# Performance work log

Measured on AMD Instinct MI355X. Metric: run time of the kernel, lower is better.

Reference implementation:

```python
import jax, jax.numpy as jnp
import numpy as np

DIM = 512; DEPTH = 2; HEADS = 8; DIM_HEAD = 64; INNER = HEADS * DIM_HEAD
MEM = 16; TOPK = 8; FF = 4 * DIM
NUM_BUCKETS = 32; MAX_DIST = 128
EPS = 1e-5


def _layernorm(x, g, b):
    m = jnp.mean(x, axis=-1, keepdims=True)
    v = jnp.var(x, axis=-1, keepdims=True)
    return (x - m) * jax.lax.rsqrt(v + EPS) * g + b


def _rel_bucket(rel_pos):
    # T5 relative-position bucketing, causal=True (as hardcoded in Encoder)
    num_buckets = NUM_BUCKETS // 2  # 16
    n = -rel_pos
    ret = (n < 0).astype(jnp.int32) * num_buckets
    n = jnp.abs(n)
    max_exact = num_buckets // 2  # 8
    is_small = n < max_exact
    nf = jnp.maximum(n, 1).astype(jnp.float32)  # safe log; masked by is_small where n==0
    val_if_large = max_exact + (
        jnp.log(nf / max_exact) / np.log(MAX_DIST / max_exact) * (num_buckets - max_exact)
    ).astype(jnp.int32)
    val_if_large = jnp.minimum(val_if_large, num_buckets - 1)
    return ret + jnp.where(is_small, n, val_if_large)


def setup_inputs() -> dict:
    key = jax.random.key(0)
    ks = jax.random.split(key, 16)
    B, N = 2, 2048
    w = lambda k, shape, s=0.02: jax.random.normal(k, shape, jnp.float32) * s
    return {
        "x": jax.random.normal(ks[0], (B, N, DIM), jnp.float32),
        "ln1_g": jnp.ones((DEPTH, DIM), jnp.float32),
        "ln1_b": jnp.zeros((DEPTH, DIM), jnp.float32),
        "Wq": w(ks[1], (DEPTH, DIM, INNER)),
        "Wkv": w(ks[2], (DEPTH, DIM, 2 * INNER)),
        "Wo": w(ks[3], (DEPTH, INNER, DIM)),
        "bo": jnp.zeros((DEPTH, DIM), jnp.float32),
        "pre_proj": w(ks[4], (DEPTH, HEADS, HEADS), 1.0),  # torch.randn init
        "mem_k": w(ks[5], (DEPTH, HEADS, MEM, DIM_HEAD), 1.0),
        "mem_v": w(ks[6], (DEPTH, HEADS, MEM, DIM_HEAD), 1.0),
        "ln2_g": jnp.ones((DEPTH, DIM), jnp.float32),
        "ln2_b": jnp.zeros((DEPTH, DIM), jnp.float32),
        "W1": w(ks[7], (DEPTH, DIM, FF)),
        "b1": jnp.zeros((DEPTH, FF), jnp.float32),
        "W2": w(ks[8], (DEPTH, FF, DIM)),
        "b2": jnp.zeros((DEPTH, DIM), jnp.float32),
        "rel_emb": w(ks[9], (NUM_BUCKETS, HEADS)),
    }


def reference(x, ln1_g, ln1_b, Wq, Wkv, Wo, bo, pre_proj, mem_k, mem_v,
              ln2_g, ln2_b, W1, b1, W2, b2, rel_emb):
    B, N, _ = x.shape
    J = N + MEM  # keys include num_mem_kv memory slots
    scale = DIM_HEAD ** -0.5
    # relative position bias, shape (1, H, N, J); same for every layer
    rel = jnp.arange(J)[None, :] - jnp.arange(N)[:, None]
    bias = jnp.transpose(rel_emb[_rel_bucket(rel)], (2, 0, 1))[None]

    for l in range(DEPTH):
        # --- PreNorm(Attention) + residual ---
        h = _layernorm(x, ln1_g[l], ln1_b[l])
        q = (h @ Wq[l]).reshape(B, N, HEADS, DIM_HEAD).transpose(0, 2, 1, 3)
        k, v = jnp.split(h @ Wkv[l], 2, axis=-1)
        k = k.reshape(B, N, HEADS, DIM_HEAD).transpose(0, 2, 1, 3)
        v = v.reshape(B, N, HEADS, DIM_HEAD).transpose(0, 2, 1, 3)
        k = jnp.concatenate([jnp.broadcast_to(mem_k[l], (B, HEADS, MEM, DIM_HEAD)), k], axis=2)
        v = jnp.concatenate([jnp.broadcast_to(mem_v[l], (B, HEADS, MEM, DIM_HEAD)), v], axis=2)
        dots = jnp.einsum('bhid,bhjd->bhij', q, k) * scale
        dots = jnp.einsum('bhij,hk->bkij', dots, pre_proj[l])  # talking heads (pre-softmax)
        dots = dots + bias
        # sparse top-k masking: keep only values >= k-th largest per row
        thr = jax.lax.top_k(dots, TOPK)[0][..., -1:]
        dots = jnp.where(dots < thr, -jnp.inf, dots)
        attn = jax.nn.softmax(dots, axis=-1)
        out = jnp.einsum('bhij,bhjd->bhid', attn, v)
        out = out.transpose(0, 2, 1, 3).reshape(B, N, INNER)
        x = out @ Wo[l] + bo[l] + x
        # --- PreNorm(FeedForward) + residual ---
        h2 = _layernorm(x, ln2_g[l], ln2_b[l])
        x = jax.nn.gelu(h2 @ W1[l] + b1[l], approximate=False) @ W2[l] + b2[l] + x
    return x
```

## Files before the change

kernel.cpp:

```cpp
#include <hip/hip_runtime.h>
#include <cmath>

typedef __bf16 bf16;
typedef __attribute__((ext_vector_type(8))) __bf16 bf16x8;
typedef __attribute__((ext_vector_type(4))) __bf16 bf16x4;
typedef __attribute__((ext_vector_type(4))) float f32x4;

#define NB 2
#define NSEQ 2048
#define NDIM 512
#define NHEADS 8
#define DHEAD 64
#define NMEM 16
#define NJ 2064
#define NJP 2176
#define NFF 2048
#define NROWS (NB*NSEQ)
#define TBL 4111

enum { EPI_QKV = 0, EPI_GELUSPLIT = 1, EPI_RESID = 2 };

__device__ __forceinline__ int xcd_swz(int bid, int n)
{
  const int cpx = n >> 3;
  return (bid & 7) * cpx + (bid >> 3);
}

template<int BM, int BN, int WAVES_M, int WAVES_N, int EPI>
__global__ __launch_bounds__(256)
void gemm_split(const bf16* __restrict__ A, const bf16* __restrict__ B,
                void* __restrict__ Cv, const float* __restrict__ bias,
                void* __restrict__ Cv2, void* __restrict__ Cv3,
                int K, int lda, int ldb, int ldc, int loA, int loB)
{
  constexpr int BK = 32;
  constexpr int WM = BM / WAVES_M;
  constexpr int WN = BN / WAVES_N;
  constexpr int MF = WM / 16;
  constexpr int NF = WN / 16;
  constexpr int AI = (BM * BK * 2) / 4096;
  constexpr int BI = (BN * BK * 2) / 4096;
  __shared__ bf16 Ash[2][BM * BK];
  __shared__ bf16 Asl[2][BM * BK];
  __shared__ bf16 Bsh[2][BN * BK];
  __shared__ bf16 Bsl[2][BN * BK];

  const int bm0 = xcd_swz(blockIdx.x, gridDim.x) * BM;
  const int bn0 = blockIdx.y * BN;
  const int t = threadIdx.x;
  const int wave = t >> 6, lane = t & 63;
  const int wr = wave / WAVES_N, wc = wave % WAVES_N;
  const int sr = t >> 2, sc = t & 3;
  const int frow = lane & 15, fk = (lane >> 4) * 8;

  auto stage = [&](int buf, int k0) {
#pragma unroll
    for (int qi = 0; qi < AI; ++qi) {
      const long long ro = (long long)(bm0 + qi * 64 + sr) * lda + (k0 + sc * 8);
      __builtin_amdgcn_global_load_lds(
          (const __attribute__((address_space(1))) void*)(A + ro),
          (__attribute__((address_space(3))) void*)(&Ash[buf][qi * 2048 + wave * 512]), 16, 0, 0);
      __builtin_amdgcn_global_load_lds(
          (const __attribute__((address_space(1))) void*)(A + ro + loA),
          (__attribute__((address_space(3))) void*)(&Asl[buf][qi * 2048 + wave * 512]), 16, 0, 0);
    }
#pragma unroll
    for (int qi = 0; qi < BI; ++qi) {
      const long long ro = (long long)(bn0 + qi * 64 + sr) * ldb + (k0 + sc * 8);
      __builtin_amdgcn_global_load_lds(
          (const __attribute__((address_space(1))) void*)(B + ro),
          (__attribute__((address_space(3))) void*)(&Bsh[buf][qi * 2048 + wave * 512]), 16, 0, 0);
      __builtin_amdgcn_global_load_lds(
          (const __attribute__((address_space(1))) void*)(B + ro + loB),
          (__attribute__((address_space(3))) void*)(&Bsl[buf][qi * 2048 + wave * 512]), 16, 0, 0);
    }
  };

  f32x4 acc[MF][NF] = {};

  stage(0, 0);
  __syncthreads();
  int cur = 0;
  for (int k0 = 0; k0 < K; k0 += BK) {
    if (k0 + BK < K) stage(cur ^ 1, k0 + BK);
    bf16x8 afh[MF], afl[MF], bfh[NF], bfl[NF];
#pragma unroll
    for (int m = 0; m < MF; m++) {
      afh[m] = *(const bf16x8*)(&Ash[cur][(wr * WM + m * 16 + frow) * BK + fk]);
      afl[m] = *(const bf16x8*)(&Asl[cur][(wr * WM + m * 16 + frow) * BK + fk]);
    }
#pragma unroll
    for (int n = 0; n < NF; n++) {
      bfh[n] = *(const bf16x8*)(&Bsh[cur][(wc * WN + n * 16 + frow) * BK + fk]);
      bfl[n] = *(const bf16x8*)(&Bsl[cur][(wc * WN + n * 16 + frow) * BK + fk]);
    }
#pragma unroll
    for (int m = 0; m < MF; m++)
#pragma unroll
      for (int n = 0; n < NF; n++) {
        acc[m][n] = __builtin_amdgcn_mfma_f32_16x16x32_bf16(afh[m], bfh[n], acc[m][n], 0, 0, 0);
        acc[m][n] = __builtin_amdgcn_mfma_f32_16x16x32_bf16(afl[m], bfh[n], acc[m][n], 0, 0, 0);
        acc[m][n] = __builtin_amdgcn_mfma_f32_16x16x32_bf16(afh[m], bfl[n], acc[m][n], 0, 0, 0);
      }
    __syncthreads();
    cur ^= 1;
  }

#pragma unroll
  for (int m = 0; m < MF; m++) {
#pragma unroll
    for (int n = 0; n < NF; n++) {
      const int row0 = bm0 + wr * WM + m * 16 + (lane >> 4) * 4;
      const int col = bn0 + wc * WN + n * 16 + (lane & 15);
#pragma unroll
      for (int r = 0; r < 4; r++) {
        const float v = acc[m][n][r];
        const long long i = row0 + r;
        if (EPI == EPI_QKV) {
          const int bb = (int)(i >> 11);
          const int il = (int)(i & 2047);
          if (col < NDIM) {
            const float vq = v * 0.125f;
            bf16* base = (bf16*)Cv;
            const long long ih = i * (long long)(2 * NDIM) + col;
            bf16 h = (bf16)vq;
            base[ih] = h;
            base[ih + NDIM] = (bf16)(vq - (float)h);
          } else if (col < 2 * NDIM) {
            bf16* ks = (bf16*)Cv3;
            const long long ih = ((long long)bb * NJP + il + NMEM) * (long long)(2 * NDIM)
                               + (col - NDIM);
            bf16 h = (bf16)v;
            ks[ih] = h;
            ks[ih + NDIM] = (bf16)(v - (float)h);
          } else {
            ((float*)Cv2)[i * (long long)NDIM + (col - 2 * NDIM)] = v;
          }
        } else if (EPI == EPI_GELUSPLIT) {
          float u = v + bias[col];
          float gl = 0.5f * u * (1.0f + erff(u * 0.7071067811865476f));
          const long long ih = i * (long long)(2 * ldc) + col;
          bf16 h = (bf16)gl;
          ((bf16*)Cv)[ih] = h;
          ((bf16*)Cv)[ih + ldc] = (bf16)(gl - (float)h);
        } else {
          float* xp = ((float*)Cv) + i * ldc + col;
          *xp = *xp + v + bias[col];
        }
      }
    }
  }
}

__global__ __launch_bounds__(256)
void s_gemm_direct(const bf16* __restrict__ Qs, const bf16* __restrict__ Ks,
                   float* __restrict__ S)
{
  const int h = blockIdx.z;
  const int bm0 = xcd_swz(blockIdx.x, gridDim.x) * 128;
  const int bn0 = blockIdx.y * 128;
  const int t = threadIdx.x;
  const int wave = t >> 6, lane = t & 63;
  const int wr = wave >> 1, wc = wave & 1;
  const int frow = lane & 15, fk = (lane >> 4) * 8;

  bf16x8 ah[4][2], al[4][2];
#pragma unroll
  for (int m = 0; m < 4; m++)
#pragma unroll
    for (int kk = 0; kk < 2; kk++) {
      const bf16* ap = Qs + (long long)(bm0 + wr * 64 + m * 16 + frow) * 1024
                     + h * 64 + kk * 32 + fk;
      ah[m][kk] = *(const bf16x8*)(ap);
      al[m][kk] = *(const bf16x8*)(ap + 512);
    }

  f32x4 acc[4][4] = {};
#pragma unroll
  for (int n = 0; n < 4; n++) {
    bf16x8 bh[2], bl[2];
#pragma unroll
    for (int kk = 0; kk < 2; kk++) {
      const bf16* bp = Ks + (long long)(bn0 + wc * 64 + n * 16 + frow) * 1024
                     + h * 64 + kk * 32 + fk;
      bh[kk] = *(const bf16x8*)(bp);
      bl[kk] = *(const bf16x8*)(bp + 512);
    }
#pragma unroll
    for (int m = 0; m < 4; m++)
#pragma unroll
      for (int kk = 0; kk < 2; kk++) {
        acc[m][n] = __builtin_amdgcn_mfma_f32_16x16x32_bf16(ah[m][kk], bh[kk], acc[m][n], 0, 0, 0);
        acc[m][n] = __builtin_amdgcn_mfma_f32_16x16x32_bf16(al[m][kk], bh[kk], acc[m][n], 0, 0, 0);
        acc[m][n] = __builtin_amdgcn_mfma_f32_16x16x32_bf16(ah[m][kk], bl[kk], acc[m][n], 0, 0, 0);
      }
  }

#pragma unroll
  for (int m = 0; m < 4; m++) {
#pragma unroll
    for (int n = 0; n < 4; n++) {
      const int row0 = bm0 + wr * 64 + m * 16 + (lane >> 4) * 4;
      const int col = bn0 + wc * 64 + n * 16 + (lane & 15);
#pragma unroll
      for (int r = 0; r < 4; r++)
        S[(long long)(row0 + r) * (NHEADS * NJP) + h * NJP + col] = acc[m][n][r];
    }
  }
}

__global__ __launch_bounds__(256)
void ln_kernel(const float* __restrict__ x, const float* __restrict__ g,
               const float* __restrict__ b, bf16* __restrict__ out)
{
  const int row = blockIdx.x * 4 + (threadIdx.x >> 6);
  const int lane = threadIdx.x & 63;
  const float* xr = x + (long long)row * NDIM;
  float4 a0 = ((const float4*)xr)[lane];
  float4 a1 = ((const float4*)xr)[lane + 64];
  float s = a0.x + a0.y + a0.z + a0.w + a1.x + a1.y + a1.z + a1.w;
  float ss = a0.x * a0.x + a0.y * a0.y + a0.z * a0.z + a0.w * a0.w
           + a1.x * a1.x + a1.y * a1.y + a1.z * a1.z + a1.w * a1.w;
#pragma unroll
  for (int d = 1; d < 64; d <<= 1) {
    s += __shfl_xor(s, d, 64);
    ss += __shfl_xor(ss, d, 64);
  }
  const float mean = s * (1.0f / NDIM);
  const float var = ss * (1.0f / NDIM) - mean * mean;
  const float rs = rsqrtf(var + 1e-5f);
  float4 g0 = ((const float4*)g)[lane], g1 = ((const float4*)g)[lane + 64];
  float4 b0 = ((const float4*)b)[lane], b1 = ((const float4*)b)[lane + 64];
  bf16* orow = out + (long long)row * (2 * NDIM);
  float y[8] = {
    (a0.x - mean) * rs * g0.x + b0.x, (a0.y - mean) * rs * g0.y + b0.y,
    (a0.z - mean) * rs * g0.z + b0.z, (a0.w - mean) * rs * g0.w + b0.w,
    (a1.x - mean) * rs * g1.x + b1.x, (a1.y - mean) * rs * g1.y + b1.y,
    (a1.z - mean) * rs * g1.z + b1.z, (a1.w - mean) * rs * g1.w + b1.w };
  bf16x4 h0, h1, l0, l1;
#pragma unroll
  for (int j = 0; j < 4; j++) {
    bf16 h = (bf16)y[j];      h0[j] = h;  l0[j] = (bf16)(y[j] - (float)h);
    bf16 h2 = (bf16)y[4 + j]; h1[j] = h2; l1[j] = (bf16)(y[4 + j] - (float)h2);
  }
  *(bf16x4*)(orow + lane * 4) = h0;
  *(bf16x4*)(orow + 256 + lane * 4) = h1;
  *(bf16x4*)(orow + 512 + lane * 4) = l0;
  *(bf16x4*)(orow + 768 + lane * 4) = l1;
}

__global__ __launch_bounds__(256)
void ks_edges(const float* __restrict__ mem_k_l, bf16* __restrict__ Ks)
{
  const int idx = blockIdx.x * 256 + threadIdx.x;
  const int c = idx & 511;
  const int jj = (idx >> 9) & 127;
  const int bb = idx >> 16;
  const int j = (jj < NMEM) ? jj : (jj - NMEM + NJ);
  float kval = 0.f;
  if (jj < NMEM) kval = mem_k_l[((c >> 6) * NMEM + jj) * DHEAD + (c & 63)];
  bf16 hv = (bf16)kval;
  const long long ro = ((long long)bb * NJP + j) * (2 * NDIM) + c;
  Ks[ro] = hv;
  Ks[ro + NDIM] = (bf16)(kval - (float)hv);
}

__global__ __launch_bounds__(512)
void mix_topk_gather(const float* __restrict__ S, const float* __restrict__ kvV,
                     const float* __restrict__ mem_v_l, const float* __restrict__ pp,
                     const float* __restrict__ table2, bf16* __restrict__ obufs,
                     int b)
{
  const int i = blockIdx.x;
  const int k = threadIdx.x >> 6;
  const int lane = threadIdx.x & 63;
  const float* srow = S + (long long)i * (NHEADS * NJP);

  float pk[8];
#pragma unroll
  for (int h = 0; h < 8; h++) pk[h] = pp[h * 8 + k];
  const float* t2k = table2 + k * TBL + (2047 - i);

  float v[34];
#pragma unroll
  for (int t = 0; t < 8; t++) {
    const int j0 = 256 * t + 4 * lane;
    v[4 * t + 0] = t2k[j0];
    v[4 * t + 1] = t2k[j0 + 1];
    v[4 * t + 2] = t2k[j0 + 2];
    v[4 * t + 3] = t2k[j0 + 3];
  }
  {
    const int j0 = 2048 + 2 * lane;
    const int jc = j0 < 2062 ? j0 : 2062;
    v[32] = t2k[jc];
    v[33] = t2k[jc + 1];
  }

#pragma unroll
  for (int h = 0; h < 8; h++) {
    const float* sp = srow + h * NJP;
    const float w = pk[h];
#pragma unroll
    for (int t = 0; t < 8; t++) {
      const float4 s4 = *(const float4*)(sp + 256 * t + 4 * lane);
      v[4 * t + 0] = fmaf(s4.x, w, v[4 * t + 0]);
      v[4 * t + 1] = fmaf(s4.y, w, v[4 * t + 1]);
      v[4 * t + 2] = fmaf(s4.z, w, v[4 * t + 2]);
      v[4 * t + 3] = fmaf(s4.w, w, v[4 * t + 3]);
    }
    const float2 s2 = *(const float2*)(sp + 2048 + 2 * lane);
    v[32] = fmaf(s2.x, w, v[32]);
    v[33] = fmaf(s2.y, w, v[33]);
  }
  {
    const int j0 = 2048 + 2 * lane;
    if (j0 >= NJ) v[32] = -1e30f;
    if (j0 + 1 >= NJ) v[33] = -1e30f;
  }

  float t8[8];
#pragma unroll
  for (int m = 0; m < 8; m++) t8[m] = -3.0e38f;
#pragma unroll
  for (int e = 0; e < 34; e++) {
    float x = v[e];
#pragma unroll
    for (int m = 0; m < 8; m++) {
      const float hi = fmaxf(t8[m], x);
      x = fminf(t8[m], x);
      t8[m] = hi;
    }
  }

#pragma unroll
  for (int d = 1; d < 64; d <<= 1) {
    float o[8], m8[8];
#pragma unroll
    for (int m = 0; m < 8; m++) o[m] = __shfl_xor(t8[m], d, 64);
#pragma unroll
    for (int m = 0; m < 8; m++) m8[m] = fmaxf(t8[m], o[7 - m]);
#define CX(a, bq) { float hi = fmaxf(m8[a], m8[bq]); float lo = fminf(m8[a], m8[bq]); m8[a] = hi; m8[bq] = lo; }
    CX(0, 4) CX(1, 5) CX(2, 6) CX(3, 7)
    CX(0, 2) CX(1, 3) CX(4, 6) CX(5, 7)
    CX(0, 1) CX(2, 3) CX(4, 5) CX(6, 7)
#undef CX
#pragma unroll
    for (int m = 0; m < 8; m++) t8[m] = m8[m];
  }
  const float mx = t8[0];
  const float thr = t8[7];
  float denom = 0.f;
#pragma unroll
  for (int m = 0; m < 8; m++) denom += __expf(t8[m] - mx);
  const float inv = 1.0f / denom;

  float acc = 0.f;
#pragma unroll
  for (int t = 0; t < 8; t++) {
#pragma unroll
    for (int e = 0; e < 4; e++) {
      unsigned long long mball = __ballot(v[t * 4 + e] >= thr);
      while (mball) {
        const int l = __builtin_ctzll(mball);
        mball &= mball - 1;
        const int jj = 256 * t + 4 * l + e;
        const float sv = __shfl(v[t * 4 + e], l);
        const float w = __expf(sv - mx) * inv;
        const float vv = (jj < NMEM)
            ? mem_v_l[(k * NMEM + jj) * DHEAD + lane]
            : kvV[(long long)(b * NSEQ + (jj - NMEM)) * NDIM + k * DHEAD + lane];
        acc = fmaf(w, vv, acc);
      }
    }
  }
#pragma unroll
  for (int e = 0; e < 2; e++) {
    unsigned long long mball = __ballot(v[32 + e] >= thr);
    while (mball) {
      const int l = __builtin_ctzll(mball);
      mball &= mball - 1;
      const int jj = 2048 + 2 * l + e;
      const float sv = __shfl(v[32 + e], l);
      const float w = __expf(sv - mx) * inv;
      const float vv = (jj < NMEM)
          ? mem_v_l[(k * NMEM + jj) * DHEAD + lane]
          : kvV[(long long)(b * NSEQ + (jj - NMEM)) * NDIM + k * DHEAD + lane];
      acc = fmaf(w, vv, acc);
    }
  }

  const long long orow = (long long)(b * NSEQ + i) * (2 * NDIM) + k * DHEAD + lane;
  bf16 h = (bf16)acc;
  obufs[orow] = h;
  obufs[orow + NDIM] = (bf16)(acc - (float)h);
}

__global__ __launch_bounds__(256)
void transpose_split(const float* __restrict__ in, bf16* __restrict__ out,
                     int R, int C)
{
  const long long idx = (long long)blockIdx.x * 256 + threadIdx.x;
  if (idx >= (long long)R * C) return;
  const int r = (int)(idx / C);
  const int c = (int)(idx % C);
  float v = in[idx];
  bf16 h = (bf16)v;
  out[(long long)c * (2 * R) + r] = h;
  out[(long long)c * (2 * R) + R + r] = (bf16)(v - (float)h);
}

__global__ __launch_bounds__(256)
void build_bias2(const float* __restrict__ rel_emb, float* __restrict__ table2)
{
  const int idx = blockIdx.x * 256 + threadIdx.x;
  if (idx >= 8 * TBL) return;
  const int k = idx / TBL;
  const int rel = (idx % TBL) - 2047;
  const int n = -rel;
  const int ret = (n < 0) ? 16 : 0;
  const int na = n < 0 ? -n : n;
  int bucket;
  if (na < 8) {
    bucket = ret + na;
  } else {
    int vl = 8 + (int)(log2((double)na * 0.125) * 2.0);
    vl = vl < 15 ? vl : 15;
    bucket = ret + vl;
  }
  table2[idx] = rel_emb[bucket * 8 + k];
}

extern "C" void kernel_launch(void* const* d_in, const int* in_sizes, int n_in,
                              void* d_out, int out_size, void* d_ws, size_t ws_size,
                              hipStream_t stream)
{
  const float* x_in    = (const float*)d_in[0];
  const float* ln1_g   = (const float*)d_in[1];
  const float* ln1_b   = (const float*)d_in[2];
  const float* Wq      = (const float*)d_in[3];
  const float* Wkv     = (const float*)d_in[4];
  const float* Wo      = (const float*)d_in[5];
  const float* bo      = (const float*)d_in[6];
  const float* pre_proj= (const float*)d_in[7];
  const float* mem_k   = (const float*)d_in[8];
  const float* mem_v   = (const float*)d_in[9];
  const float* ln2_g   = (const float*)d_in[10];
  const float* ln2_b   = (const float*)d_in[11];
  const float* W1      = (const float*)d_in[12];
  const float* b1      = (const float*)d_in[13];
  const float* W2      = (const float*)d_in[14];
  const float* b2      = (const float*)d_in[15];
  const float* rel_emb = (const float*)d_in[16];

  char* p = (char*)d_ws;
  auto alloc = [&](size_t bytes) -> char* {
    char* r = p;
    p += (bytes + 255) & ~(size_t)255;
    return r;
  };

  float* x    = (float*)alloc((size_t)NROWS * NDIM * 4);
  char*  RA   = alloc((size_t)NROWS * 2 * NDIM * 2);
  bf16*  hs    = (bf16*)RA;
  bf16*  obufs = (bf16*)RA;
  char*  RB   = alloc((size_t)NROWS * 2 * NFF * 2);
  bf16*  Qs    = (bf16*)RB;
  bf16*  Ks    = (bf16*)(RB + (size_t)NROWS * 2 * NDIM * 2);
  bf16*  tbufs = (bf16*)RB;
  float* kvV  = (float*)alloc((size_t)NROWS * NDIM * 4);
  float* S    = (float*)alloc((size_t)NSEQ * NHEADS * NJP * 4);
  bf16*  WqkvT= (bf16*)alloc((size_t)2 * 3 * NDIM * 2 * NDIM * 2);
  bf16*  WoT  = (bf16*)alloc((size_t)2 * NDIM * 2 * NDIM * 2);
  bf16*  W1T  = (bf16*)alloc((size_t)2 * NFF * 2 * NDIM * 2);
  bf16*  W2T  = (bf16*)alloc((size_t)2 * NDIM * 2 * NFF * 2);
  float* table2= (float*)alloc((size_t)8 * TBL * 4);

  hipMemcpyAsync(x, x_in, (size_t)NROWS * NDIM * 4, hipMemcpyDeviceToDevice, stream);
  build_bias2<<<(8 * TBL + 255) / 256, 256, 0, stream>>>(rel_emb, table2);
  for (int l = 0; l < 2; l++) {
    bf16* WqkvT_l = WqkvT + (size_t)l * 3 * NDIM * 2 * NDIM;
    transpose_split<<<(NDIM * NDIM + 255) / 256, 256, 0, stream>>>(
        Wq + (size_t)l * NDIM * NDIM, WqkvT_l, NDIM, NDIM);
    transpose_split<<<(2 * NDIM * NDIM + 255) / 256, 256, 0, stream>>>(
        Wkv + (size_t)l * NDIM * 2 * NDIM, WqkvT_l + (size_t)NDIM * 2 * NDIM,
        NDIM, 2 * NDIM);
    transpose_split<<<(NDIM * NDIM + 255) / 256, 256, 0, stream>>>(
        Wo + (size_t)l * NDIM * NDIM, WoT + (size_t)l * NDIM * 2 * NDIM, NDIM, NDIM);
    transpose_split<<<(NDIM * NFF + 255) / 256, 256, 0, stream>>>(
        W1 + (size_t)l * NDIM * NFF, W1T + (size_t)l * NFF * 2 * NDIM, NDIM, NFF);
    transpose_split<<<(NFF * NDIM + 255) / 256, 256, 0, stream>>>(
        W2 + (size_t)l * NFF * NDIM, W2T + (size_t)l * NDIM * 2 * NFF, NFF, NDIM);
  }

  for (int l = 0; l < 2; l++) {
    const bf16* WqkvT_l = WqkvT + (size_t)l * 3 * NDIM * 2 * NDIM;
    const bf16* WoT_l  = WoT + (size_t)l * NDIM * 2 * NDIM;
    const bf16* W1T_l  = W1T + (size_t)l * NFF * 2 * NDIM;
    const bf16* W2T_l  = W2T + (size_t)l * NDIM * 2 * NFF;
    const float* mem_v_l = mem_v + (size_t)l * NHEADS * NMEM * DHEAD;

    ln_kernel<<<NROWS / 4, 256, 0, stream>>>(x, ln1_g + l * NDIM, ln1_b + l * NDIM, hs);
    gemm_split<128, 128, 2, 2, EPI_QKV><<<dim3(NROWS / 128, 12), 256, 0, stream>>>(
        hs, WqkvT_l, Qs, nullptr, kvV, Ks, NDIM, 2 * NDIM, 2 * NDIM, 0, NDIM, NDIM);
    ks_edges<<<(2 * 128 * 512) / 256, 256, 0, stream>>>(
        mem_k + (size_t)l * NHEADS * NMEM * DHEAD, Ks);

    for (int b = 0; b < NB; b++) {
      s_gemm_direct<<<dim3(NSEQ / 128, NJP / 128, NHEADS), 256, 0, stream>>>(
          Qs + (long long)b * NSEQ * 1024, Ks + (long long)b * NJP * 1024, S);
      mix_topk_gather<<<NSEQ, 512, 0, stream>>>(
          S, kvV, mem_v_l, pre_proj + l * 64, table2, obufs, b);
    }

    gemm_split<128, 64, 2, 2, EPI_RESID><<<dim3(NROWS / 128, NDIM / 64), 256, 0, stream>>>(
        obufs, WoT_l, x, bo + l * NDIM, nullptr, nullptr,
        NDIM, 2 * NDIM, 2 * NDIM, NDIM, NDIM, NDIM);

    ln_kernel<<<NROWS / 4, 256, 0, stream>>>(x, ln2_g + l * NDIM, ln2_b + l * NDIM, hs);
    gemm_split<128, 128, 2, 2, EPI_GELUSPLIT><<<dim3(NROWS / 128, NFF / 128), 256, 0, stream>>>(
        hs, W1T_l, tbufs, b1 + l * NFF, nullptr, nullptr,
        NDIM, 2 * NDIM, 2 * NDIM, NFF, NDIM, NDIM);
    gemm_split<128, 64, 2, 2, EPI_RESID><<<dim3(NROWS / 128, NDIM / 64), 256, 0, stream>>>(
        tbufs, W2T_l, x, b2 + l * NDIM, nullptr, nullptr,
        NFF, 2 * NFF, 2 * NFF, NDIM, NFF, NFF);
  }

  hipMemcpyAsync(d_out, x, (size_t)out_size * 4, hipMemcpyDeviceToDevice, stream);
}
```

Baseline: 889.8 us.

## Fuse QK^T score GEMM with talking-heads mix and top-k into one kernel

```diff
diff --git a/kernel.cpp b/kernel.cpp
--- a/kernel.cpp
+++ b/kernel.cpp
@@ -17,6 +17,7 @@
 #define NFF 2048
 #define NROWS (NB*NSEQ)
 #define TBL 4111
+#define JQ 544
 
 enum { EPI_QKV = 0, EPI_GELUSPLIT = 1, EPI_RESID = 2 };
 
@@ -152,61 +153,186 @@
   }
 }
 
-__global__ __launch_bounds__(256)
-void s_gemm_direct(const bf16* __restrict__ Qs, const bf16* __restrict__ Ks,
-                   float* __restrict__ S)
-{
-  const int h = blockIdx.z;
-  const int bm0 = xcd_swz(blockIdx.x, gridDim.x) * 128;
-  const int bn0 = blockIdx.y * 128;
-  const int t = threadIdx.x;
-  const int wave = t >> 6, lane = t & 63;
-  const int wr = wave >> 1, wc = wave & 1;
+__global__ __launch_bounds__(512)
+void attn_fused(const bf16* __restrict__ Qs, const bf16* __restrict__ Ks,
+                const float* __restrict__ pp, const float* __restrict__ table2,
+                float* __restrict__ cand_v, int* __restrict__ cand_i)
+{
+  __shared__ float sS[8 * 64 * 36];
+  const int it = blockIdx.x;
+  const int q  = blockIdx.y;
+  const int b  = blockIdx.z;
+  const int wv = threadIdx.x >> 6;
+  const int lane = threadIdx.x & 63;
+  const int i0 = it * 64;
+  const int jq0 = q * JQ;
+
+  const bf16* Qb = Qs + ((long long)b * NSEQ + i0) * 1024;
+  const bf16* Kb = Ks + (long long)b * NJP * 1024;
   const int frow = lane & 15, fk = (lane >> 4) * 8;
 
   bf16x8 ah[4][2], al[4][2];
 #pragma unroll
   for (int m = 0; m < 4; m++)
 #pragma unroll
-    for (int kk = 0; kk < 2; kk++) {
-      const bf16* ap = Qs + (long long)(bm0 + wr * 64 + m * 16 + frow) * 1024
-                     + h * 64 + kk * 32 + fk;
-      ah[m][kk] = *(const bf16x8*)(ap);
-      al[m][kk] = *(const bf16x8*)(ap + 512);
-    }
-
-  f32x4 acc[4][4] = {};
-#pragma unroll
-  for (int n = 0; n < 4; n++) {
-    bf16x8 bh[2], bl[2];
-#pragma unroll
-    for (int kk = 0; kk < 2; kk++) {
-      const bf16* bp = Ks + (long long)(bn0 + wc * 64 + n * 16 + frow) * 1024
-                     + h * 64 + kk * 32 + fk;
-      bh[kk] = *(const bf16x8*)(bp);
-      bl[kk] = *(const bf16x8*)(bp + 512);
-    }
+    for (int ks = 0; ks < 2; ks++) {
+      const bf16* ap = Qb + (long long)(m * 16 + frow) * 1024 + wv * 64 + ks * 32 + fk;
+      ah[m][ks] = *(const bf16x8*)(ap);
+      al[m][ks] = *(const bf16x8*)(ap + 512);
+    }
+
+  float pk[8];
+#pragma unroll
+  for (int h = 0; h < 8; h++) pk[h] = pp[h * 8 + wv];
+  const float* t2l = table2 + wv * TBL + 2047 - (i0 + lane);
+
+  float t8[8]; int i8[8];
+#pragma unroll
+  for (int m = 0; m < 8; m++) { t8[m] = -3.0e38f; i8[m] = 0; }
+
+  bf16x8 bh[2][2], bl[2][2];
+  auto loadB = [&](int st) {
+    const int j0 = jq0 + st * 32;
+#pragma unroll
+    for (int n = 0; n < 2; n++)
+#pragma unroll
+      for (int ks = 0; ks < 2; ks++) {
+        const bf16* bp = Kb + (long long)(j0 + n * 16 + frow) * 1024 + wv * 64 + ks * 32 + fk;
+        bh[n][ks] = *(const bf16x8*)(bp);
+        bl[n][ks] = *(const bf16x8*)(bp + 512);
+      }
+  };
+  loadB(0);
+
+  for (int st = 0; st < 17; ++st) {
+    f32x4 acc[4][2] = {};
+#pragma unroll
+    for (int n = 0; n < 2; n++)
+#pragma unroll
+      for (int m = 0; m < 4; m++)
+#pragma unroll
+        for (int ks = 0; ks < 2; ks++) {
+          acc[m][n] = __builtin_amdgcn_mfma_f32_16x16x32_bf16(ah[m][ks], bh[n][ks], acc[m][n], 0, 0, 0);
+          acc[m][n] = __builtin_amdgcn_mfma_f32_16x16x32_bf16(al[m][ks], bh[n][ks], acc[m][n], 0, 0, 0);
+          acc[m][n] = __builtin_amdgcn_mfma_f32_16x16x32_bf16(ah[m][ks], bl[n][ks], acc[m][n], 0, 0, 0);
+        }
 #pragma unroll
     for (int m = 0; m < 4; m++)
 #pragma unroll
-      for (int kk = 0; kk < 2; kk++) {
-        acc[m][n] = __builtin_amdgcn_mfma_f32_16x16x32_bf16(ah[m][kk], bh[kk], acc[m][n], 0, 0, 0);
-        acc[m][n] = __builtin_amdgcn_mfma_f32_16x16x32_bf16(al[m][kk], bh[kk], acc[m][n], 0, 0, 0);
-        acc[m][n] = __builtin_amdgcn_mfma_f32_16x16x32_bf16(ah[m][kk], bl[kk], acc[m][n], 0, 0, 0);
+      for (int n = 0; n < 2; n++)
+#pragma unroll
+        for (int r = 0; r < 4; r++)
+          sS[wv * 2304 + (m * 16 + (lane >> 4) * 4 + r) * 36 + n * 16 + (lane & 15)] = acc[m][n][r];
+    __syncthreads();
+
+    if (st < 16) loadB(st + 1);
+
+#pragma unroll
+    for (int s = 0; s < 8; ++s) {
+      const int jl = s * 4;
+      const int jg = jq0 + st * 32 + jl;
+      float v[4];
+#pragma unroll
+      for (int e = 0; e < 4; e++) {
+        const int jr = (jg + e < NJ) ? (jg + e) : (NJ - 1);
+        v[e] = t2l[jr];
       }
-  }
-
-#pragma unroll
-  for (int m = 0; m < 4; m++) {
-#pragma unroll
-    for (int n = 0; n < 4; n++) {
-      const int row0 = bm0 + wr * 64 + m * 16 + (lane >> 4) * 4;
-      const int col = bn0 + wc * 64 + n * 16 + (lane & 15);
-#pragma unroll
-      for (int r = 0; r < 4; r++)
-        S[(long long)(row0 + r) * (NHEADS * NJP) + h * NJP + col] = acc[m][n][r];
-    }
-  }
+#pragma unroll
+      for (int h = 0; h < 8; h++) {
+        const float4 s4 = *(const float4*)(sS + h * 2304 + lane * 36 + jl);
+        v[0] = fmaf(s4.x, pk[h], v[0]);
+        v[1] = fmaf(s4.y, pk[h], v[1]);
+        v[2] = fmaf(s4.z, pk[h], v[2]);
+        v[3] = fmaf(s4.w, pk[h], v[3]);
+      }
+#pragma unroll
+      for (int e = 0; e < 4; e++) {
+        if (jg + e >= NJ) v[e] = -1e30f;
+        const float x = v[e];
+        if (x > t8[7]) {
+          t8[7] = x; i8[7] = jg + e;
+#pragma unroll
+          for (int m = 6; m >= 0; m--)
+            if (t8[m + 1] > t8[m]) {
+              float tv = t8[m]; t8[m] = t8[m + 1]; t8[m + 1] = tv;
+              int ti = i8[m]; i8[m] = i8[m + 1]; i8[m + 1] = ti;
+            }
+        }
+      }
+    }
+    __syncthreads();
+  }
+
+  const long long cb = (((long long)(b * NSEQ + i0 + lane)) * NHEADS + wv) * 32 + q * 8;
+#pragma unroll
+  for (int m = 0; m < 8; m++) {
+    cand_v[cb + m] = t8[m];
+    cand_i[cb + m] = i8[m];
+  }
+}
+
+__global__ __launch_bounds__(512)
+void merge_gather(const float* __restrict__ cand_v, const int* __restrict__ cand_i,
+                  const float* __restrict__ kvV, const float* __restrict__ mem_v_l,
+                  bf16* __restrict__ obufs)
+{
+  const int i = blockIdx.x;
+  const int b = blockIdx.y;
+  const int k = threadIdx.x >> 6;
+  const int lane = threadIdx.x & 63;
+  const long long cbase = (((long long)(b * NSEQ + i)) * NHEADS + k) * 32;
+
+  float cv = -3.0e38f;
+  int ci = 0;
+  if (lane < 32) {
+    cv = cand_v[cbase + lane];
+    ci = cand_i[cbase + lane];
+  }
+
+  float t8[8];
+  t8[0] = cv;
+#pragma unroll
+  for (int m = 1; m < 8; m++) t8[m] = -3.0e38f;
+#pragma unroll
+  for (int d = 1; d < 64; d <<= 1) {
+    float o[8], m8[8];
+#pragma unroll
+    for (int m = 0; m < 8; m++) o[m] = __shfl_xor(t8[m], d, 64);
+#pragma unroll
+    for (int m = 0; m < 8; m++) m8[m] = fmaxf(t8[m], o[7 - m]);
+#define CX(a, bq) { float hi = fmaxf(m8[a], m8[bq]); float lo = fminf(m8[a], m8[bq]); m8[a] = hi; m8[bq] = lo; }
+    CX(0, 4) CX(1, 5) CX(2, 6) CX(3, 7)
+    CX(0, 2) CX(1, 3) CX(4, 6) CX(5, 7)
+    CX(0, 1) CX(2, 3) CX(4, 5) CX(6, 7)
+#undef CX
+#pragma unroll
+    for (int m = 0; m < 8; m++) t8[m] = m8[m];
+  }
+  const float mx = t8[0];
+  const float thr = t8[7];
+  float denom = 0.f;
+#pragma unroll
+  for (int m = 0; m < 8; m++) denom += __expf(t8[m] - mx);
+  const float inv = 1.0f / denom;
+
+  float acc = 0.f;
+  unsigned long long mball = __ballot(cv >= thr);
+  while (mball) {
+    const int l = __builtin_ctzll(mball);
+    mball &= mball - 1;
+    const int jj = __shfl(ci, l);
+    const float sv = __shfl(cv, l);
+    const float w = __expf(sv - mx) * inv;
+    const float vv = (jj < NMEM)
+        ? mem_v_l[(k * NMEM + jj) * DHEAD + lane]
+        : kvV[(long long)(b * NSEQ + (jj - NMEM)) * NDIM + k * DHEAD + lane];
+    acc = fmaf(w, vv, acc);
+  }
+
+  const long long orow = (long long)(b * NSEQ + i) * (2 * NDIM) + k * DHEAD + lane;
+  bf16 h = (bf16)acc;
+  obufs[orow] = h;
+  obufs[orow + NDIM] = (bf16)(acc - (float)h);
 }
 
 __global__ __launch_bounds__(256)
@@ -263,137 +389,6 @@
   const long long ro = ((long long)bb * NJP + j) * (2 * NDIM) + c;
   Ks[ro] = hv;
   Ks[ro + NDIM] = (bf16)(kval - (float)hv);
-}
-
-__global__ __launch_bounds__(512)
-void mix_topk_gather(const float* __restrict__ S, const float* __restrict__ kvV,
-                     const float* __restrict__ mem_v_l, const float* __restrict__ pp,
-                     const float* __restrict__ table2, bf16* __restrict__ obufs,
-                     int b)
-{
-  const int i = blockIdx.x;
-  const int k = threadIdx.x >> 6;
-  const int lane = threadIdx.x & 63;
-  const float* srow = S + (long long)i * (NHEADS * NJP);
-
-  float pk[8];
-#pragma unroll
-  for (int h = 0; h < 8; h++) pk[h] = pp[h * 8 + k];
-  const float* t2k = table2 + k * TBL + (2047 - i);
-
-  float v[34];
-#pragma unroll
-  for (int t = 0; t < 8; t++) {
-    const int j0 = 256 * t + 4 * lane;
-    v[4 * t + 0] = t2k[j0];
-    v[4 * t + 1] = t2k[j0 + 1];
-    v[4 * t + 2] = t2k[j0 + 2];
-    v[4 * t + 3] = t2k[j0 + 3];
-  }
-  {
-    const int j0 = 2048 + 2 * lane;
-    const int jc = j0 < 2062 ? j0 : 2062;
-    v[32] = t2k[jc];
-    v[33] = t2k[jc + 1];
-  }
-
-#pragma unroll
-  for (int h = 0; h < 8; h++) {
-    const float* sp = srow + h * NJP;
-    const float w = pk[h];
-#pragma unroll
-    for (int t = 0; t < 8; t++) {
-      const float4 s4 = *(const float4*)(sp + 256 * t + 4 * lane);
-      v[4 * t + 0] = fmaf(s4.x, w, v[4 * t + 0]);
-      v[4 * t + 1] = fmaf(s4.y, w, v[4 * t + 1]);
-      v[4 * t + 2] = fmaf(s4.z, w, v[4 * t + 2]);
-      v[4 * t + 3] = fmaf(s4.w, w, v[4 * t + 3]);
-    }
-    const float2 s2 = *(const float2*)(sp + 2048 + 2 * lane);
-    v[32] = fmaf(s2.x, w, v[32]);
-    v[33] = fmaf(s2.y, w, v[33]);
-  }
-  {
-    const int j0 = 2048 + 2 * lane;
-    if (j0 >= NJ) v[32] = -1e30f;
-    if (j0 + 1 >= NJ) v[33] = -1e30f;
-  }
-
-  float t8[8];
-#pragma unroll
-  for (int m = 0; m < 8; m++) t8[m] = -3.0e38f;
-#pragma unroll
-  for (int e = 0; e < 34; e++) {
-    float x = v[e];
-#pragma unroll
-    for (int m = 0; m < 8; m++) {
-      const float hi = fmaxf(t8[m], x);
-      x = fminf(t8[m], x);
-      t8[m] = hi;
-    }
-  }
-
-#pragma unroll
-  for (int d = 1; d < 64; d <<= 1) {
-    float o[8], m8[8];
-#pragma unroll
-    for (int m = 0; m < 8; m++) o[m] = __shfl_xor(t8[m], d, 64);
-#pragma unroll
-    for (int m = 0; m < 8; m++) m8[m] = fmaxf(t8[m], o[7 - m]);
-#define CX(a, bq) { float hi = fmaxf(m8[a], m8[bq]); float lo = fminf(m8[a], m8[bq]); m8[a] = hi; m8[bq] = lo; }
-    CX(0, 4) CX(1, 5) CX(2, 6) CX(3, 7)
-    CX(0, 2) CX(1, 3) CX(4, 6) CX(5, 7)
-    CX(0, 1) CX(2, 3) CX(4, 5) CX(6, 7)
-#undef CX
-#pragma unroll
-    for (int m = 0; m < 8; m++) t8[m] = m8[m];
-  }
-  const float mx = t8[0];
-  const float thr = t8[7];
-  float denom = 0.f;
-#pragma unroll
-  for (int m = 0; m < 8; m++) denom += __expf(t8[m] - mx);
-  const float inv = 1.0f / denom;
-
-  float acc = 0.f;
-#pragma unroll
-  for (int t = 0; t < 8; t++) {
-#pragma unroll
-    for (int e = 0; e < 4; e++) {
-      unsigned long long mball = __ballot(v[t * 4 + e] >= thr);
-      while (mball) {
-        const int l = __builtin_ctzll(mball);
-        mball &= mball - 1;
-        const int jj = 256 * t + 4 * l + e;
-        const float sv = __shfl(v[t * 4 + e], l);
-        const float w = __expf(sv - mx) * inv;
-        const float vv = (jj < NMEM)
-            ? mem_v_l[(k * NMEM + jj) * DHEAD + lane]
-            : kvV[(long long)(b * NSEQ + (jj - NMEM)) * NDIM + k * DHEAD + lane];
-        acc = fmaf(w, vv, acc);
-      }
-    }
-  }
-#pragma unroll
-  for (int e = 0; e < 2; e++) {
-    unsigned long long mball = __ballot(v[32 + e] >= thr);
-    while (mball) {
-      const int l = __builtin_ctzll(mball);
-      mball &= mball - 1;
-      const int jj = 2048 + 2 * l + e;
-      const float sv = __shfl(v[32 + e], l);
-      const float w = __expf(sv - mx) * inv;
-      const float vv = (jj < NMEM)
-          ? mem_v_l[(k * NMEM + jj) * DHEAD + lane]
-          : kvV[(long long)(b * NSEQ + (jj - NMEM)) * NDIM + k * DHEAD + lane];
-      acc = fmaf(w, vv, acc);
-    }
-  }
-
-  const long long orow = (long long)(b * NSEQ + i) * (2 * NDIM) + k * DHEAD + lane;
-  bf16 h = (bf16)acc;
-  obufs[orow] = h;
-  obufs[orow + NDIM] = (bf16)(acc - (float)h);
 }
 
 __global__ __launch_bounds__(256)
@@ -469,7 +464,8 @@
   bf16*  Ks    = (bf16*)(RB + (size_t)NROWS * 2 * NDIM * 2);
   bf16*  tbufs = (bf16*)RB;
   float* kvV  = (float*)alloc((size_t)NROWS * NDIM * 4);
-  float* S    = (float*)alloc((size_t)NSEQ * NHEADS * NJP * 4);
+  float* cand_v = (float*)alloc((size_t)NB * NSEQ * NHEADS * 32 * 4);
+  int*   cand_i = (int*)  alloc((size_t)NB * NSEQ * NHEADS * 32 * 4);
   bf16*  WqkvT= (bf16*)alloc((size_t)2 * 3 * NDIM * 2 * NDIM * 2);
   bf16*  WoT  = (bf16*)alloc((size_t)2 * NDIM * 2 * NDIM * 2);
   bf16*  W1T  = (bf16*)alloc((size_t)2 * NFF * 2 * NDIM * 2);
@@ -506,12 +502,10 @@
     ks_edges<<<(2 * 128 * 512) / 256, 256, 0, stream>>>(
         mem_k + (size_t)l * NHEADS * NMEM * DHEAD, Ks);
 
-    for (int b = 0; b < NB; b++) {
-      s_gemm_direct<<<dim3(NSEQ / 128, NJP / 128, NHEADS), 256, 0, stream>>>(
-          Qs + (long long)b * NSEQ * 1024, Ks + (long long)b * NJP * 1024, S);
-      mix_topk_gather<<<NSEQ, 512, 0, stream>>>(
-          S, kvV, mem_v_l, pre_proj + l * 64, table2, obufs, b);
-    }
+    attn_fused<<<dim3(NSEQ / 64, 4, NB), 512, 0, stream>>>(
+        Qs, Ks, pre_proj + l * 64, table2, cand_v, cand_i);
+    merge_gather<<<dim3(NSEQ, NB), 512, 0, stream>>>(
+        cand_v, cand_i, kvV, mem_v_l, obufs);
 
     gemm_split<128, 64, 2, 2, EPI_RESID><<<dim3(NROWS / 128, NDIM / 64), 256, 0, stream>>>(
         obufs, WoT_l, x, bo + l * NDIM, nullptr, nullptr,
```

Result: slower. 1.004 ms (+12.8%).
